# Performance work log

Hardware: AMD Instinct MI355X
Metric: run time of the kernel (lower is better)

Reference implementation:

```python
import jax, jax.numpy as jnp
import numpy as np

NEG = -1e30  # effective -inf in float32, safe under logaddexp grads
EPS = 1e-7   # keras.backend.epsilon()


def _ctc_loss(y_pred, y_true):
    """Faithful port of keras.backend.ctc_batch_cost with full-length
    input_length=T and label_length=L (as the CTCLayer sets them).
    y_pred: [B, T, C] post-softmax probabilities; blank = C-1.
    y_true: [B, L] int labels in [0, C-1).
    Returns loss [B, 1].
    """
    logp = jnp.log(y_pred + EPS)            # keras takes log(prob + eps)
    B, T, C = y_pred.shape
    L = y_true.shape[1]
    S = 2 * L + 1
    blank = C - 1

    # Extended label sequence: blank, l1, blank, l2, ..., blank  -> [B, S]
    ext = jnp.full((B, S), blank, dtype=y_true.dtype).at[:, 1::2].set(y_true)
    # Per-time emission log-probs of extended symbols: [B, T, S]
    lp_ext = jnp.take_along_axis(logp, ext[:, None, :], axis=2)

    # Skip transition s-2 -> s allowed when ext[s] != blank and ext[s] != ext[s-2]
    prev2_ext = jnp.pad(ext[:, :-2], ((0, 0), (2, 0)), constant_values=-1)
    allow_skip = (ext != blank) & (ext != prev2_ext)  # [B, S]

    # alpha init at t=0
    alpha = jnp.full((B, S), NEG, dtype=logp.dtype)
    alpha = alpha.at[:, 0].set(lp_ext[:, 0, 0]).at[:, 1].set(lp_ext[:, 0, 1])

    def step(alpha, lp_t):
        shift1 = jnp.pad(alpha[:, :-1], ((0, 0), (1, 0)), constant_values=NEG)
        shift2 = jnp.pad(alpha[:, :-2], ((0, 0), (2, 0)), constant_values=NEG)
        shift2 = jnp.where(allow_skip, shift2, NEG)
        new = jnp.logaddexp(jnp.logaddexp(alpha, shift1), shift2) + lp_t
        return new, None

    lp_seq = jnp.moveaxis(lp_ext[:, 1:, :], 1, 0)  # [T-1, B, S]
    alpha, _ = jax.lax.scan(step, alpha, lp_seq)

    # Terminate in final blank or final label
    loss = -jnp.logaddexp(alpha[:, S - 1], alpha[:, S - 2])  # [B]
    return loss[:, None]  # keras returns [B, 1]


def setup_inputs() -> dict:
    key = jax.random.key(0)
    k1, k2 = jax.random.split(key)
    B, T, C, L = 256, 256, 1000, 64
    y_true = jax.random.randint(k1, (B, L), 0, C - 1, dtype=jnp.int64)
    logits = jax.random.normal(k2, (B, T, C), dtype=jnp.float32)
    y_pred = jax.nn.softmax(logits, axis=-1)  # module expects softmax probs
    return {"y_true": y_true, "y_pred": y_pred}


def reference(y_true, y_pred):
    return _ctc_loss(y_pred, y_true)
```

## Files before the change

### kernel.cpp

```cpp
#include <hip/hip_runtime.h>


#define T_    256
#define C_    1000
#define L_    64
#define BLANK 999
#define NEGF  (-1e30f)
#define EPSF  (1e-7f)
#define RS    66
#define PD    8

__global__ __launch_bounds__(256)
void ctc_gather_kernel(const int* __restrict__ y_true,
                       const float* __restrict__ y_pred,
                       float* __restrict__ lp) {
    const int wave = threadIdx.x >> 6;
    const int lane = threadIdx.x & 63;
    const int pair = blockIdx.x * 4 + wave;
    const int b = pair >> 8;
    const int t = pair & 255;

    const int lab = y_true[b * L_ + lane];
    const float* __restrict__ row = y_pred + (size_t)pair * C_;
    float* __restrict__ orow = lp + (size_t)pair * RS;

    float v = row[lab];
    orow[1 + lane] = __logf(v + EPSF);
    if (lane == 0) {
        orow[0] = __logf(row[BLANK] + EPSF);
    }
}

__global__ __launch_bounds__(64)
void ctc_scan_kernel(const int* __restrict__ y_true,
                     const float* __restrict__ lp,
                     float* __restrict__ out) {
    const int b    = blockIdx.x;
    const int lane = threadIdx.x;

    const float* __restrict__ lrow = lp + (size_t)b * T_ * RS;

    const int lab   = y_true[b * L_ + lane];
    const int labm1 = __shfl_up(lab, 1, 64);
    const bool allow = (lane > 0) && (lab != labm1);

    float aE = (lane == 0) ? lrow[0] : NEGF;
    float aO = (lane == 0) ? lrow[1] : NEGF;
    float aL = NEGF;

    float pB[PD], pL[PD];
    #pragma unroll
    for (int k = 0; k < PD; ++k) {
        int t = 1 + k; if (t > T_ - 1) t = T_ - 1;
        pB[k] = lrow[t * RS];
        pL[k] = lrow[t * RS + 1 + lane];
    }

    for (int tb = 1; tb < T_; tb += PD) {
        #pragma unroll
        for (int j = 0; j < PD; ++j) {
            const int t = tb + j;
            if (t >= T_) break;

            int tn = t + PD; if (tn > T_ - 1) tn = T_ - 1;
            float nB = lrow[tn * RS];
            float nL = lrow[tn * RS + 1 + lane];

            const float lpB = pB[j];
            const float lpL = pL[j];

            float upO = __shfl_up(aO, 1, 64);
            if (lane == 0) upO = NEGF;

            float mE = fmaxf(aE, upO);
            float nE = mE + __logf(__expf(aE - mE) + __expf(upO - mE)) + lpB;

            float sk = allow ? upO : NEGF;
            float mO = fmaxf(fmaxf(aO, aE), sk);
            float nO = mO + __logf(__expf(aO - mO) + __expf(aE - mO) +
                                   __expf(sk - mO)) + lpL;

            float mL = fmaxf(aL, aO);
            float nL2 = mL + __logf(__expf(aL - mL) + __expf(aO - mL)) + lpB;

            aE = nE; aO = nO; aL = nL2;
            pB[j] = nB; pL[j] = nL;
        }
    }

    if (lane == 63) {
        float m = fmaxf(aL, aO);
        out[b] = -(m + __logf(__expf(aL - m) + __expf(aO - m)));
    }
}

extern "C" void kernel_launch(void* const* d_in, const int* in_sizes, int n_in,
                              void* d_out, int out_size, void* d_ws, size_t ws_size,
                              hipStream_t stream) {
    const int*   y_true = (const int*)d_in[0];
    const float* y_pred = (const float*)d_in[1];
    float*       out    = (float*)d_out;
    float*       lp     = (float*)d_ws;
    (void)in_sizes; (void)n_in; (void)ws_size; (void)out_size;

    ctc_gather_kernel<<<dim3((256 * 256) / 4), dim3(256), 0, stream>>>(y_true, y_pred, lp);
    ctc_scan_kernel<<<dim3(256), dim3(64), 0, stream>>>(y_true, lp, out);
}
```

Baseline: 405.8 us.

## Stage scan emission chunks through double-buffered LDS with float4 global loads

The scan kernel now bulk-loads 64-timestep chunks of the gathered log-prob workspace with coalesced float4 loads into registers. It writes them to a double-buffered shared-memory array and scans from LDS, prefetching the next chunk while the current one is processed. This replaces per-step scattered global loads that sat on the serial recurrence's latency path. The row stride is padded from 66 to 68 floats for float4 alignment, which adds a little extra workspace traffic, and the large register arrays raise register pressure.

```diff
diff --git a/kernel.cpp b/kernel.cpp
--- a/kernel.cpp
+++ b/kernel.cpp
@@ -7,8 +7,9 @@
 #define BLANK 999
 #define NEGF  (-1e30f)
 #define EPSF  (1e-7f)
-#define RS    66
-#define PD    8
+#define RS    68
+#define CK    64
+#define NV    17
 
 __global__ __launch_bounds__(256)
 void ctc_gather_kernel(const int* __restrict__ y_true,
@@ -18,7 +19,6 @@
     const int lane = threadIdx.x & 63;
     const int pair = blockIdx.x * 4 + wave;
     const int b = pair >> 8;
-    const int t = pair & 255;
 
     const int lab = y_true[b * L_ + lane];
     const float* __restrict__ row = y_pred + (size_t)pair * C_;
@@ -35,6 +35,8 @@
 void ctc_scan_kernel(const int* __restrict__ y_true,
                      const float* __restrict__ lp,
                      float* __restrict__ out) {
+    __shared__ float sbuf[2][CK * RS];
+
     const int b    = blockIdx.x;
     const int lane = threadIdx.x;
 
@@ -44,49 +46,63 @@
     const int labm1 = __shfl_up(lab, 1, 64);
     const bool allow = (lane > 0) && (lab != labm1);
 
-    float aE = (lane == 0) ? lrow[0] : NEGF;
-    float aO = (lane == 0) ? lrow[1] : NEGF;
-    float aL = NEGF;
+    float aE = NEGF, aO = NEGF, aL = NEGF;
 
-    float pB[PD], pL[PD];
-    #pragma unroll
-    for (int k = 0; k < PD; ++k) {
-        int t = 1 + k; if (t > T_ - 1) t = T_ - 1;
-        pB[k] = lrow[t * RS];
-        pL[k] = lrow[t * RS + 1 + lane];
-    }
+    float4 va[NV], vb[NV];
 
-    for (int tb = 1; tb < T_; tb += PD) {
+    auto loadChunk = [&](int c, float4 (&v)[NV]) {
+        const float4* g = (const float4*)(lrow + (size_t)c * CK * RS);
         #pragma unroll
-        for (int j = 0; j < PD; ++j) {
-            const int t = tb + j;
-            if (t >= T_) break;
+        for (int k = 0; k < NV; ++k) v[k] = g[k * 64 + lane];
+    };
+    auto writeChunk = [&](int sel, float4 (&v)[NV]) {
+        float4* d = (float4*)&sbuf[sel][0];
+        #pragma unroll
+        for (int k = 0; k < NV; ++k) d[k * 64 + lane] = v[k];
+    };
 
-            int tn = t + PD; if (tn > T_ - 1) tn = T_ - 1;
-            float nB = lrow[tn * RS];
-            float nL = lrow[tn * RS + 1 + lane];
+    auto step = [&](float lpB, float lpL) {
+        float upO = __shfl_up(aO, 1, 64);
+        if (lane == 0) upO = NEGF;
+        float mE = fmaxf(aE, upO);
+        float nE = mE + __logf(__expf(aE - mE) + __expf(upO - mE)) + lpB;
+        float sk = allow ? upO : NEGF;
+        float mO = fmaxf(fmaxf(aO, aE), sk);
+        float nO = mO + __logf(__expf(aO - mO) + __expf(aE - mO) +
+                               __expf(sk - mO)) + lpL;
+        float mL = fmaxf(aL, aO);
+        float nL2 = mL + __logf(__expf(aL - mL) + __expf(aO - mL)) + lpB;
+        aE = nE; aO = nO; aL = nL2;
+    };
 
-            const float lpB = pB[j];
-            const float lpL = pL[j];
+    auto scanChunk = [&](int sel, int rlo) {
+        const float* B = &sbuf[sel][0];
+        float rB0 = B[rlo * RS],       rL0 = B[rlo * RS + 1 + lane];
+        float rB1 = B[(rlo + 1) * RS], rL1 = B[(rlo + 1) * RS + 1 + lane];
+        for (int j = rlo; j < CK; ++j) {
+            float lpB = rB0, lpL = rL0;
+            rB0 = rB1; rL0 = rL1;
+            int nr = j + 2; if (nr > CK - 1) nr = CK - 1;
+            rB1 = B[nr * RS]; rL1 = B[nr * RS + 1 + lane];
+            step(lpB, lpL);
+        }
+    };
 
-            float upO = __shfl_up(aO, 1, 64);
-            if (lane == 0) upO = NEGF;
+    loadChunk(0, va); writeChunk(0, va);
+    loadChunk(1, vb);
 
-            float mE = fmaxf(aE, upO);
-            float nE = mE + __logf(__expf(aE - mE) + __expf(upO - mE)) + lpB;
+    aE = (lane == 0) ? sbuf[0][0] : NEGF;
+    aO = (lane == 0) ? sbuf[0][1] : NEGF;
 
-            float sk = allow ? upO : NEGF;
-            float mO = fmaxf(fmaxf(aO, aE), sk);
-            float nO = mO + __logf(__expf(aO - mO) + __expf(aE - mO) +
-                                   __expf(sk - mO)) + lpL;
-
-            float mL = fmaxf(aL, aO);
-            float nL2 = mL + __logf(__expf(aL - mL) + __expf(aO - mL)) + lpB;
-
-            aE = nE; aO = nO; aL = nL2;
-            pB[j] = nB; pL[j] = nL;
-        }
-    }
+    scanChunk(0, 1);
+    writeChunk(1, vb);
+    loadChunk(2, va);
+    scanChunk(1, 0);
+    writeChunk(0, va);
+    loadChunk(3, vb);
+    scanChunk(0, 0);
+    writeChunk(1, vb);
+    scanChunk(1, 0);
 
     if (lane == 63) {
         float m = fmaxf(aL, aO);
```

Result: no change. 401.2 us (-1.1%).

## Switch CTC forward recursion to scaled linear probability space with LDS staging

Applied to the files above, without the earlier changes.

The alpha recursion now works in linear probability space with multiply-add instead of log-sum-exp. Every 8 steps it rescales by the wave-wide maximum and accumulates the log of that factor, which removes the many exp/log calls on the serial critical path. The gather kernel now stores prob+eps instead of its log, and each batch's strip is bulk-loaded into shared memory (via global_load_lds when available) before the scan. The trade-offs are the risk of underflow between rescalings when probabilities are tiny, a cross-lane max reduction every 8 steps, and 68 KB of shared memory per block.

```diff
diff --git a/kernel.cpp b/kernel.cpp
--- a/kernel.cpp
+++ b/kernel.cpp
@@ -5,92 +5,101 @@
 #define C_    1000
 #define L_    64
 #define BLANK 999
-#define NEGF  (-1e30f)
 #define EPSF  (1e-7f)
-#define RS    66
-#define PD    8
+#define RS    68
+#define NCHUNK ((T_ * RS) / 256)
 
 __global__ __launch_bounds__(256)
 void ctc_gather_kernel(const int* __restrict__ y_true,
                        const float* __restrict__ y_pred,
-                       float* __restrict__ lp) {
+                       float* __restrict__ V) {
     const int wave = threadIdx.x >> 6;
     const int lane = threadIdx.x & 63;
     const int pair = blockIdx.x * 4 + wave;
     const int b = pair >> 8;
-    const int t = pair & 255;
 
     const int lab = y_true[b * L_ + lane];
     const float* __restrict__ row = y_pred + (size_t)pair * C_;
-    float* __restrict__ orow = lp + (size_t)pair * RS;
+    float* __restrict__ orow = V + (size_t)pair * RS;
 
-    float v = row[lab];
-    orow[1 + lane] = __logf(v + EPSF);
-    if (lane == 0) {
-        orow[0] = __logf(row[BLANK] + EPSF);
-    }
+    orow[1 + lane] = row[lab] + EPSF;
+    if (lane == 0) orow[0] = row[BLANK] + EPSF;
 }
 
 __global__ __launch_bounds__(64)
 void ctc_scan_kernel(const int* __restrict__ y_true,
-                     const float* __restrict__ lp,
+                     const float* __restrict__ V,
                      float* __restrict__ out) {
+    __shared__ float sb[T_ * RS];
+
     const int b    = blockIdx.x;
     const int lane = threadIdx.x;
 
-    const float* __restrict__ lrow = lp + (size_t)b * T_ * RS;
+    const float* __restrict__ strip = V + (size_t)b * T_ * RS;
+
+#if __has_builtin(__builtin_amdgcn_global_load_lds)
+    typedef const __attribute__((address_space(1))) float gfloat;
+    typedef __attribute__((address_space(3))) float sfloat;
+    #pragma unroll
+    for (int k = 0; k < NCHUNK; ++k) {
+        __builtin_amdgcn_global_load_lds((gfloat*)(strip + k * 256 + lane * 4),
+                                         (sfloat*)(sb + k * 256), 16, 0, 0);
+    }
+    asm volatile("s_waitcnt vmcnt(0)" ::: "memory");
+#else
+    #pragma unroll
+    for (int k = 0; k < NCHUNK; ++k)
+        ((float4*)sb)[k * 64 + lane] = ((const float4*)strip)[k * 64 + lane];
+    __syncthreads();
+#endif
 
     const int lab   = y_true[b * L_ + lane];
     const int labm1 = __shfl_up(lab, 1, 64);
     const bool allow = (lane > 0) && (lab != labm1);
 
-    float aE = (lane == 0) ? lrow[0] : NEGF;
-    float aO = (lane == 0) ? lrow[1] : NEGF;
-    float aL = NEGF;
+    float aE = 0.f, aO = 0.f, aL = 0.f, lsum = 0.f;
+    if (lane == 0) { aE = sb[0]; aO = sb[1]; }
 
-    float pB[PD], pL[PD];
+    float rB[4], rL[4];
     #pragma unroll
-    for (int k = 0; k < PD; ++k) {
-        int t = 1 + k; if (t > T_ - 1) t = T_ - 1;
-        pB[k] = lrow[t * RS];
-        pL[k] = lrow[t * RS + 1 + lane];
+    for (int k = 0; k < 4; ++k) {
+        rB[k] = sb[(1 + k) * RS];
+        rL[k] = sb[(1 + k) * RS + 1 + lane];
     }
 
-    for (int tb = 1; tb < T_; tb += PD) {
+    for (int t0 = 1; t0 < T_; t0 += 4) {
         #pragma unroll
-        for (int j = 0; j < PD; ++j) {
-            const int t = tb + j;
+        for (int j = 0; j < 4; ++j) {
+            const int t = t0 + j;
             if (t >= T_) break;
-
-            int tn = t + PD; if (tn > T_ - 1) tn = T_ - 1;
-            float nB = lrow[tn * RS];
-            float nL = lrow[tn * RS + 1 + lane];
-
-            const float lpB = pB[j];
-            const float lpL = pL[j];
+            const float pB = rB[j], pL = rL[j];
+            int tn = t + 4; if (tn > T_ - 1) tn = T_ - 1;
+            rB[j] = sb[tn * RS];
+            rL[j] = sb[tn * RS + 1 + lane];
 
             float upO = __shfl_up(aO, 1, 64);
-            if (lane == 0) upO = NEGF;
+            if (lane == 0) upO = 0.f;
 
-            float mE = fmaxf(aE, upO);
-            float nE = mE + __logf(__expf(aE - mE) + __expf(upO - mE)) + lpB;
+            const float nE = (aE + upO) * pB;
+            const float sk = allow ? upO : 0.f;
+            const float nO = (aO + aE + sk) * pL;
+            const float nL = (aL + aO) * pB;
+            aE = nE; aO = nO; aL = nL;
 
-            float sk = allow ? upO : NEGF;
-            float mO = fmaxf(fmaxf(aO, aE), sk);
-            float nO = mO + __logf(__expf(aO - mO) + __expf(aE - mO) +
-                                   __expf(sk - mO)) + lpL;
-
-            float mL = fmaxf(aL, aO);
-            float nL2 = mL + __logf(__expf(aL - mL) + __expf(aO - mL)) + lpB;
-
-            aE = nE; aO = nO; aL = nL2;
-            pB[j] = nB; pL[j] = nL;
+            if ((t & 7) == 0) {
+                float m = fmaxf(fmaxf(aE, aO), aL);
+                #pragma unroll
+                for (int d = 1; d < 64; d <<= 1)
+                    m = fmaxf(m, __shfl_xor(m, d, 64));
+                const float r = __builtin_amdgcn_rcpf(m);
+                aE *= r; aO *= r; aL *= r;
+                lsum += __logf(m);
+            }
         }
     }
 
     if (lane == 63) {
-        float m = fmaxf(aL, aO);
-        out[b] = -(m + __logf(__expf(aL - m) + __expf(aO - m)));
+        out[b] = -(__logf(aL + aO) + lsum);
     }
 }
 
@@ -100,9 +109,9 @@
     const int*   y_true = (const int*)d_in[0];
     const float* y_pred = (const float*)d_in[1];
     float*       out    = (float*)d_out;
-    float*       lp     = (float*)d_ws;
+    float*       V      = (float*)d_ws;
     (void)in_sizes; (void)n_in; (void)ws_size; (void)out_size;
 
-    ctc_gather_kernel<<<dim3((256 * 256) / 4), dim3(256), 0, stream>>>(y_true, y_pred, lp);
-    ctc_scan_kernel<<<dim3(256), dim3(64), 0, stream>>>(y_true, lp, out);
+    ctc_gather_kernel<<<dim3((256 * T_) / 4), dim3(256), 0, stream>>>(y_true, y_pred, V);
+    ctc_scan_kernel<<<dim3(256), dim3(64), 0, stream>>>(y_true, V, out);
 }
```

Result: faster. 374.7 us (-7.7%).
